# Optimization experiments

Measured on AMD Instinct MI355X. Metric: run time of the kernel, lower is better.

Reference implementation:

```python
import jax, jax.numpy as jnp
import numpy as np

B, NPG, H, D = 8, 6250, 4, 128   # graphs, nodes/graph, heads, hidden
N = B * NPG                       # 50000 nodes total
E = 400000                        # edges
VOCAB = 10000


def setup_inputs() -> dict:
    key = jax.random.key(0)
    ks = jax.random.split(key, 12)
    p = lambda k, shape: jax.random.normal(k, shape, dtype=jnp.float32) * 0.05
    return {
        "node_ids": jax.random.randint(ks[0], (N,), 0, VOCAB),
        "src": jax.random.randint(ks[1], (E,), 0, N),
        "dst": jax.random.randint(ks[2], (E,), 0, N),
        "emb": p(ks[3], (VOCAB, D)),
        "W_src": p(ks[4], (D, H * D)), "b_src": jnp.zeros((H * D,), jnp.float32),
        "W_dst": p(ks[5], (D, H * D)), "b_dst": jnp.zeros((H * D,), jnp.float32),
        "attn": p(ks[6], (H, D)),
        "W_res": p(ks[7], (D, H * D)), "b_res": jnp.zeros((H * D,), jnp.float32),
        "W_gc": p(ks[8], (D, D)), "b_gc": jnp.zeros((D,), jnp.float32),
        "W_mlp": p(ks[9], (3 * D, 1)), "b_mlp": jnp.zeros((1,), jnp.float32),
    }


def _leaky(x, s):
    return jnp.where(x >= 0, x, s * x)


def _maxpool(feat):
    # dgl.max_nodes: per-graph max over nodes -> [B, feat_dim]
    return jnp.max(feat.reshape(B, NPG, -1), axis=1)


def _gatv2(x, src, dst, W_src, b_src, W_dst, b_dst, attn, W_res, b_res):
    # DGL GATv2Conv (share_weights=False, residual=True, eval mode -> no dropout)
    hs = (x @ W_src + b_src).reshape(N, H, D)
    hd = (x @ W_dst + b_dst).reshape(N, H, D)
    e = _leaky(hs[src] + hd[dst], 0.2)              # [E,H,D]
    logits = jnp.einsum('ehd,hd->eh', e, attn)      # [E,H]
    m = jax.ops.segment_max(logits, dst, num_segments=N)
    ex = jnp.exp(logits - m[dst])
    denom = jax.ops.segment_sum(ex, dst, num_segments=N)
    alpha = ex / denom[dst]                          # edge softmax per dst/head
    rst = jax.ops.segment_sum(hs[src] * alpha[..., None], dst, num_segments=N)
    rst = rst + (x @ W_res + b_res).reshape(N, H, D)
    return _leaky(rst, 0.01)                         # nn.LeakyReLU() activation


def _graphconv(x, src, dst, W, b):
    # DGL GraphConv norm='both', allow_zero_in_degree=True, LeakyReLU activation
    ones = jnp.ones((E,), x.dtype)
    dout = jnp.clip(jax.ops.segment_sum(ones, src, num_segments=N), 1.0, None)
    din = jnp.clip(jax.ops.segment_sum(ones, dst, num_segments=N), 1.0, None)
    h = x * jax.lax.rsqrt(dout)[:, None]
    agg = jax.ops.segment_sum(h[src], dst, num_segments=N)
    h = agg * jax.lax.rsqrt(din)[:, None]
    return _leaky(h @ W + b, 0.01)


def reference(node_ids, src, dst, emb, W_src, b_src, W_dst, b_dst, attn,
              W_res, b_res, W_gc, b_gc, W_mlp, b_mlp):
    feat = emb[node_ids]                             # featurize_nodes
    pools = [_maxpool(feat)]
    res = _gatv2(feat, src, dst, W_src, b_src, W_dst, b_dst, attn,
                 W_res, b_res).mean(axis=1)          # mean over heads -> [N,D]
    pools.append(_maxpool(res))
    res = _graphconv(res, src, dst, W_gc, b_gc)
    pools.append(_maxpool(res))
    agg = jnp.concatenate(pools, axis=1)             # [B, 3D]
    # reward_predictor_block_two: ReLU -> (Dropout eval) -> Linear(3D, 1)
    return jax.nn.relu(agg) @ W_mlp + b_mlp          # BCE logits [B,1]
```

## Files before the change

kernel.cpp:

```cpp
#include <hip/hip_runtime.h>
#include <float.h>
#include <math.h>

#define Bg   8
#define NPGc 6250
#define Hh   4
#define Dd   128
#define Nn   50000
#define Ee   400000
#define HDd  512
#define NCHUNK 49

typedef unsigned short ushort_t;
typedef __attribute__((ext_vector_type(8))) short bf16x8;
typedef __attribute__((ext_vector_type(4))) float f32x4;
typedef __attribute__((ext_vector_type(2))) float f32x2;

__device__ __forceinline__ void atomicMaxF(float* addr, float val) {
    if (val >= 0.0f) atomicMax((int*)addr, __float_as_int(val));
    else             atomicMin((unsigned int*)addr, __float_as_uint(val));
}

__device__ __forceinline__ ushort_t f2bf(float x) {
    unsigned u = __float_as_uint(x);
    unsigned r = (u + 0x7FFFu + ((u >> 16) & 1u)) >> 16;
    return (ushort_t)r;
}

__device__ __forceinline__ f32x2 bfpair(unsigned u) {
    f32x2 r;
    r.x = __uint_as_float(u << 16);
    r.y = __uint_as_float(u & 0xFFFF0000u);
    return r;
}

__global__ void setup_kernel(const int* __restrict__ ids, const float* __restrict__ emb,
                             float* __restrict__ feat, ushort_t* __restrict__ feat_bf,
                             const float* __restrict__ W_src, const float* __restrict__ W_dst,
                             const float* __restrict__ W_res, const float* __restrict__ W_gc,
                             const float* __restrict__ b_src, const float* __restrict__ b_dst,
                             const float* __restrict__ b_res,
                             ushort_t* __restrict__ Wt_s, ushort_t* __restrict__ Wt_dr,
                             ushort_t* __restrict__ Wt_gc,
                             float* __restrict__ bias_s, float* __restrict__ bias_dr,
                             int* __restrict__ din_i, float* __restrict__ dout,
                             int* __restrict__ cursor, float* __restrict__ pools) {
    int i = blockIdx.x * blockDim.x + threadIdx.x;
    {
        int n = i >> 5, c = i & 31;
        int id = ids[n];
        float4 v = ((const float4*)emb)[(size_t)id * 32 + c];
        ((float4*)feat)[(size_t)n * 32 + c] = v;
        ushort4 b;
        b.x = f2bf(v.x); b.y = f2bf(v.y); b.z = f2bf(v.z); b.w = f2bf(v.w);
        ((ushort4*)feat_bf)[(size_t)n * 32 + c] = b;
    }
    if (i < Nn) { din_i[i] = 0; dout[i] = 0.0f; cursor[i] = 0; }
    if (i < Bg * 3 * Dd) pools[i] = -FLT_MAX;
    if (i < 512 * 128) {
        int c = i >> 7, k = i & 127;
        Wt_s[i] = f2bf(W_src[k * 512 + c]);
    } else if (i < 512 * 128 + 1024 * 128) {
        int j = i - 512 * 128;
        int c = j >> 7, k = j & 127;
        float v = (c < 512) ? W_dst[k * 512 + c] : W_res[k * 512 + (c - 512)];
        Wt_dr[j] = f2bf(v);
    } else if (i < 512 * 128 + 1024 * 128 + 128 * 128) {
        int j = i - (512 * 128 + 1024 * 128);
        int c = j >> 7, k = j & 127;
        Wt_gc[j] = f2bf(W_gc[k * 128 + c]);
    }
    if (i < 512) bias_s[i] = b_src[i];
    if (i < 1024) bias_dr[i] = (i < 512) ? b_dst[i] : b_res[i - 512];
}

__global__ void maxpool_kernel(const float* __restrict__ x, float* __restrict__ pools, int col_off) {
    int b = blockIdx.x, chunk = blockIdx.y, d = threadIdx.x;
    int i0 = chunk * 125, i1 = i0 + 125;
    float mx = -FLT_MAX;
    for (int i = i0; i < i1; ++i)
        mx = fmaxf(mx, x[((size_t)(b * NPGc + i)) * Dd + d]);
    atomicMaxF(&pools[b * (3 * Dd) + col_off + d], mx);
}

__global__ void maxpool_bf_kernel(const ushort_t* __restrict__ x, float* __restrict__ pools, int col_off) {
    int b = blockIdx.x, chunk = blockIdx.y, lane = threadIdx.x;
    int i0 = chunk * 125;
    f32x2 mx = {-FLT_MAX, -FLT_MAX};
    for (int i = 0; i < 125; ++i) {
        unsigned u = *(const unsigned*)(x + ((size_t)(b * NPGc + i0 + i)) * Dd + lane * 2);
        mx = __builtin_elementwise_max(mx, bfpair(u));
    }
    atomicMaxF(&pools[b * (3 * Dd) + col_off + lane * 2],     mx.x);
    atomicMaxF(&pools[b * (3 * Dd) + col_off + lane * 2 + 1], mx.y);
}

template<int GNT, int NCS>
__global__ __launch_bounds__(256) void mfma_gemm_kernel(
    const ushort_t* __restrict__ A, const ushort_t* __restrict__ Wt,
    const float* __restrict__ bias, ushort_t* __restrict__ Ob,
    int n_rows, int WN)
{
    __shared__ ushort_t Cs[2][64 * 64];
    int bid = blockIdx.x;
    int lin = (bid & 7) * (gridDim.x >> 3) + (bid >> 3);
    int row0 = (lin / NCS) * 64;
    int ct0  = (lin % NCS) * GNT;
    int w = threadIdx.x >> 6, lane = threadIdx.x & 63;
    int lrow = lane & 15, kg = lane >> 4;

    bf16x8 av[4][4];
    {
        const ushort_t* ap = A + (size_t)(row0 + lrow) * 128 + kg * 8;
        #pragma unroll
        for (int fi = 0; fi < 4; ++fi)
            #pragma unroll
            for (int ks = 0; ks < 4; ++ks)
                av[fi][ks] = *(const bf16x8*)(ap + fi * 16 * 128 + ks * 32);
    }
    bf16x8 wv[GNT][4];
    float4 bv[GNT];
    {
        const ushort_t* wp = Wt + (size_t)(ct0 * 64 + w * 16 + lrow) * 128 + kg * 8;
        #pragma unroll
        for (int ct = 0; ct < GNT; ++ct) {
            #pragma unroll
            for (int ks = 0; ks < 4; ++ks)
                wv[ct][ks] = *(const bf16x8*)(wp + (size_t)ct * 8192 + ks * 32);
            bv[ct] = *(const float4*)(bias + (ct0 + ct) * 64 + w * 16 + kg * 4);
        }
    }

    #pragma unroll
    for (int ct = 0; ct < GNT; ++ct) {
        f32x4 acc[4] = {};
        #pragma unroll
        for (int ks = 0; ks < 4; ++ks)
            #pragma unroll
            for (int fi = 0; fi < 4; ++fi)
                acc[fi] = __builtin_amdgcn_mfma_f32_16x16x32_bf16(wv[ct][ks], av[fi][ks], acc[fi], 0, 0, 0);

        ushort_t* cb = Cs[ct & 1];
        int cbase = w * 32 + kg * 8;
        #pragma unroll
        for (int fi = 0; fi < 4; ++fi) {
            float o0 = acc[fi][0] + bv[ct].x;
            float o1 = acc[fi][1] + bv[ct].y;
            float o2 = acc[fi][2] + bv[ct].z;
            float o3 = acc[fi][3] + bv[ct].w;
            unsigned q0, q1;
            asm("v_cvt_pk_bf16_f32 %0, %1, %2" : "=v"(q0) : "v"(o0), "v"(o1));
            asm("v_cvt_pk_bf16_f32 %0, %1, %2" : "=v"(q1) : "v"(o2), "v"(o3));
            int r = fi * 16 + lrow;
            int cbyte = cbase ^ ((r & 7) << 4);
            uint2 q; q.x = q0; q.y = q1;
            *(uint2*)((char*)cb + r * 128 + cbyte) = q;
        }
        __syncthreads();
        {
            int t = threadIdx.x;
            const char* cbr = (const char*)cb;
            #pragma unroll
            for (int h = 0; h < 2; ++h) {
                int r  = (h * 256 + t) >> 3;
                int ch = t & 7;
                int cbyte = (ch * 16) ^ ((r & 7) << 4);
                uint4 v = *(const uint4*)(cbr + r * 128 + cbyte);
                int grow = row0 + r;
                if (grow < n_rows)
                    *(uint4*)((char*)Ob + ((size_t)grow * WN + (ct0 + ct) * 64) * 2 + ch * 16) = v;
            }
        }
    }
}

__global__ __launch_bounds__(256) void mfma_gc_pool_kernel(
    const ushort_t* __restrict__ A, const ushort_t* __restrict__ Wt,
    const float* __restrict__ bias, float* __restrict__ pools)
{
    int g = blockIdx.x / 98, lb = blockIdx.x % 98;
    int row0 = g * NPGc + lb * 64;
    int w = threadIdx.x >> 6, lane = threadIdx.x & 63;
    int lrow = lane & 15, kg = lane >> 4;

    bf16x8 av[4][4];
    {
        const ushort_t* ap = A + (size_t)(row0 + lrow) * 128 + kg * 8;
        #pragma unroll
        for (int fi = 0; fi < 4; ++fi)
            #pragma unroll
            for (int ks = 0; ks < 4; ++ks)
                av[fi][ks] = *(const bf16x8*)(ap + fi * 16 * 128 + ks * 32);
    }

    #pragma unroll
    for (int ct = 0; ct < 2; ++ct) {
        bf16x8 wv[4];
        const ushort_t* wp = Wt + (size_t)(ct * 64 + w * 16 + lrow) * 128 + kg * 8;
        #pragma unroll
        for (int ks = 0; ks < 4; ++ks) wv[ks] = *(const bf16x8*)(wp + ks * 32);

        f32x4 acc[4] = {};
        #pragma unroll
        for (int ks = 0; ks < 4; ++ks)
            #pragma unroll
            for (int fi = 0; fi < 4; ++fi)
                acc[fi] = __builtin_amdgcn_mfma_f32_16x16x32_bf16(wv[ks], av[fi][ks], acc[fi], 0, 0, 0);

        int colb = ct * 64 + w * 16 + kg * 4;
        float4 bv4 = *(const float4*)(bias + colb);
        float mcol[4] = {-FLT_MAX, -FLT_MAX, -FLT_MAX, -FLT_MAX};
        #pragma unroll
        for (int fi = 0; fi < 4; ++fi) {
            int lr = lb * 64 + fi * 16 + lrow;
            bool valid = lr < NPGc;
            #pragma unroll
            for (int j = 0; j < 4; ++j) {
                float v = acc[fi][j] + ((const float*)&bv4)[j];
                v = v >= 0.0f ? v : 0.01f * v;
                if (valid) mcol[j] = fmaxf(mcol[j], v);
            }
        }
        #pragma unroll
        for (int j = 0; j < 4; ++j) {
            mcol[j] = fmaxf(mcol[j], __shfl_xor(mcol[j], 1));
            mcol[j] = fmaxf(mcol[j], __shfl_xor(mcol[j], 2));
            mcol[j] = fmaxf(mcol[j], __shfl_xor(mcol[j], 4));
            mcol[j] = fmaxf(mcol[j], __shfl_xor(mcol[j], 8));
        }
        if (lrow == 0) {
            #pragma unroll
            for (int j = 0; j < 4; ++j)
                atomicMaxF(&pools[g * (3 * Dd) + 2 * Dd + colb + j], mcol[j]);
        }
    }
}

__global__ void degree2_kernel(const int* __restrict__ src, const int* __restrict__ dst,
                               int* __restrict__ din_i, float* __restrict__ dout) {
    int e = blockIdx.x * blockDim.x + threadIdx.x;
    if (e >= Ee) return;
    atomicAdd(&din_i[dst[e]], 1);
    atomicAdd(&dout[src[e]], 1.0f);
}

__global__ __launch_bounds__(256) void scan_reduce_kernel(const int* __restrict__ din_i,
                                                          int* __restrict__ partials) {
    int b = blockIdx.x, t = threadIdx.x;
    int base = b * 1024 + t * 4;
    int s = 0;
    #pragma unroll
    for (int j = 0; j < 4; ++j) { int i = base + j; if (i < Nn) s += din_i[i]; }
    #pragma unroll
    for (int off = 32; off > 0; off >>= 1) s += __shfl_xor(s, off);
    __shared__ int wsum[4];
    if ((t & 63) == 0) wsum[t >> 6] = s;
    __syncthreads();
    if (t == 0) partials[b] = wsum[0] + wsum[1] + wsum[2] + wsum[3];
}

__global__ void scan_mid_kernel(int* __restrict__ partials, int* __restrict__ row_start) {
    if (threadIdx.x == 0) {
        int acc = 0;
        for (int i = 0; i < NCHUNK; ++i) { int v = partials[i]; partials[i] = acc; acc += v; }
        row_start[Nn] = acc;
    }
}

__global__ __launch_bounds__(256) void scan_final_kernel(const int* __restrict__ din_i,
                                                         const int* __restrict__ partials,
                                                         int* __restrict__ row_start,
                                                         float* __restrict__ din_f) {
    int b = blockIdx.x, t = threadIdx.x;
    int base = b * 1024 + t * 4;
    int v[4]; int s = 0;
    #pragma unroll
    for (int j = 0; j < 4; ++j) {
        v[j] = (base + j < Nn) ? din_i[base + j] : 0;
        s += v[j];
    }
    __shared__ int buf[256];
    buf[t] = s;
    __syncthreads();
    #pragma unroll
    for (int off = 1; off < 256; off <<= 1) {
        int x = (t >= off) ? buf[t - off] : 0;
        __syncthreads();
        buf[t] += x;
        __syncthreads();
    }
    int excl = buf[t] - s + partials[b];
    #pragma unroll
    for (int j = 0; j < 4; ++j) {
        if (base + j < Nn) {
            row_start[base + j] = excl;
            din_f[base + j] = (float)v[j];
            excl += v[j];
        }
    }
}

__global__ void scatter_kernel(const int* __restrict__ src, const int* __restrict__ dst,
                               const int* __restrict__ row_start, int* __restrict__ cursor,
                               int* __restrict__ csr_src) {
    int e = blockIdx.x * blockDim.x + threadIdx.x;
    if (e >= Ee) return;
    int d = dst[e];
    int slot = row_start[d] + atomicAdd(&cursor[d], 1);
    csr_src[slot] = src[e];
}

__global__ __launch_bounds__(256) void gat_fused_kernel(
    const ushort_t* __restrict__ feat_bf, const ushort_t* __restrict__ hs,
    const ushort_t* __restrict__ Wt_dr, const float* __restrict__ bias_dr,
    const float* __restrict__ attn,
    const int* __restrict__ row_start, const int* __restrict__ csr_src,
    ushort_t* __restrict__ res_bf)
{
    __shared__ char HD[16 * 2048];
    int nb = blockIdx.x * 16;
    int w = threadIdx.x >> 6, lane = threadIdx.x & 63;
    int lrow = lane & 15, kg = lane >> 4;

    {
        bf16x8 av[4];
        const ushort_t* ap = feat_bf + (size_t)(nb + lrow) * 128 + kg * 8;
        #pragma unroll
        for (int ks = 0; ks < 4; ++ks) av[ks] = *(const bf16x8*)(ap + ks * 32);
        #pragma unroll 4
        for (int cf = 0; cf < 16; ++cf) {
            int col0 = w * 256 + cf * 16;
            bf16x8 wv[4];
            const ushort_t* wp = Wt_dr + (size_t)(col0 + lrow) * 128 + kg * 8;
            #pragma unroll
            for (int ks = 0; ks < 4; ++ks) wv[ks] = *(const bf16x8*)(wp + ks * 32);
            f32x4 acc = {};
            #pragma unroll
            for (int ks = 0; ks < 4; ++ks)
                acc = __builtin_amdgcn_mfma_f32_16x16x32_bf16(wv[ks], av[ks], acc, 0, 0, 0);
            int colb = col0 + kg * 4;
            float4 bv = *(const float4*)(bias_dr + colb);
            float o0 = acc[0] + bv.x, o1 = acc[1] + bv.y;
            float o2 = acc[2] + bv.z, o3 = acc[3] + bv.w;
            unsigned q0, q1;
            asm("v_cvt_pk_bf16_f32 %0, %1, %2" : "=v"(q0) : "v"(o0), "v"(o1));
            asm("v_cvt_pk_bf16_f32 %0, %1, %2" : "=v"(q1) : "v"(o2), "v"(o3));
            int byte = (colb * 2) ^ ((lrow & 7) << 4);
            uint2 q; q.x = q0; q.y = q1;
            *(uint2*)(HD + lrow * 2048 + byte) = q;
        }
    }
    __syncthreads();

    const f32x2 z2 = {0.0f, 0.0f};
    f32x2 at0, at1, at2, at3;
    {
        float4 a0 = *(const float4*)(attn + lane * 8);
        float4 a1 = *(const float4*)(attn + lane * 8 + 4);
        at0.x = a0.x; at0.y = a0.y; at1.x = a0.z; at1.y = a0.w;
        at2.x = a1.x; at2.y = a1.y; at3.x = a1.z; at3.y = a1.w;
    }

    for (int i = 0; i < 4; ++i) {
        int r = w * 4 + i;
        int d = nb + r;
        int e0 = row_start[d], e1 = row_start[d + 1];

        f32x2 hd0, hd1, hd2, hd3;
        {
            uint4 hr = *(const uint4*)(HD + r * 2048 + ((lane * 16) ^ ((r & 7) << 4)));
            hd0 = bfpair(hr.x); hd1 = bfpair(hr.y); hd2 = bfpair(hr.z); hd3 = bfpair(hr.w);
        }

        float denom = 0.0f;
        f32x2 ac0 = z2, ac1 = z2, ac2 = z2, ac3 = z2;

#define LOGIT_PRE(rr, h0, h1, h2, h3, pout)                                           \
    {                                                                                 \
        h0 = bfpair(rr.x); h1 = bfpair(rr.y); h2 = bfpair(rr.z); h3 = bfpair(rr.w);   \
        f32x2 p2 = z2;                                                                \
        { f32x2 x = h0 + hd0;                                                         \
          p2 += (__builtin_elementwise_max(x, z2) + 0.2f * __builtin_elementwise_min(x, z2)) * at0; } \
        { f32x2 x = h1 + hd1;                                                         \
          p2 += (__builtin_elementwise_max(x, z2) + 0.2f * __builtin_elementwise_min(x, z2)) * at1; } \
        { f32x2 x = h2 + hd2;                                                         \
          p2 += (__builtin_elementwise_max(x, z2) + 0.2f * __builtin_elementwise_min(x, z2)) * at2; } \
        { f32x2 x = h3 + hd3;                                                         \
          p2 += (__builtin_elementwise_max(x, z2) + 0.2f * __builtin_elementwise_min(x, z2)) * at3; } \
        pout = p2.x + p2.y;                                                           \
    }

        int e = e0;
        for (; e + 4 <= e1; e += 4) {
            int sA = csr_src[e], sB = csr_src[e + 1], sC = csr_src[e + 2], sD = csr_src[e + 3];
            uint4 rA = *(const uint4*)(hs + (size_t)sA * HDd + lane * 8);
            uint4 rB = *(const uint4*)(hs + (size_t)sB * HDd + lane * 8);
            uint4 rC = *(const uint4*)(hs + (size_t)sC * HDd + lane * 8);
            uint4 rD = *(const uint4*)(hs + (size_t)sD * HDd + lane * 8);
            f32x2 hA0, hA1, hA2, hA3, hB0, hB1, hB2, hB3;
            f32x2 hC0, hC1, hC2, hC3, hD0, hD1, hD2, hD3;
            float pA, pB, pC, pD;
            LOGIT_PRE(rA, hA0, hA1, hA2, hA3, pA);
            LOGIT_PRE(rB, hB0, hB1, hB2, hB3, pB);
            LOGIT_PRE(rC, hC0, hC1, hC2, hC3, pC);
            LOGIT_PRE(rD, hD0, hD1, hD2, hD3, pD);
            pA += __shfl_xor(pA, 1); pB += __shfl_xor(pB, 1); pC += __shfl_xor(pC, 1); pD += __shfl_xor(pD, 1);
            pA += __shfl_xor(pA, 2); pB += __shfl_xor(pB, 2); pC += __shfl_xor(pC, 2); pD += __shfl_xor(pD, 2);
            pA += __shfl_xor(pA, 4); pB += __shfl_xor(pB, 4); pC += __shfl_xor(pC, 4); pD += __shfl_xor(pD, 4);
            pA += __shfl_xor(pA, 8); pB += __shfl_xor(pB, 8); pC += __shfl_xor(pC, 8); pD += __shfl_xor(pD, 8);
            float exA = __expf(fminf(fmaxf(pA, -40.0f), 40.0f));
            float exB = __expf(fminf(fmaxf(pB, -40.0f), 40.0f));
            float exC = __expf(fminf(fmaxf(pC, -40.0f), 40.0f));
            float exD = __expf(fminf(fmaxf(pD, -40.0f), 40.0f));
            denom += (exA + exB) + (exC + exD);
            ac0 += hA0 * exA + hB0 * exB + hC0 * exC + hD0 * exD;
            ac1 += hA1 * exA + hB1 * exB + hC1 * exC + hD1 * exD;
            ac2 += hA2 * exA + hB2 * exB + hC2 * exC + hD2 * exD;
            ac3 += hA3 * exA + hB3 * exB + hC3 * exC + hD3 * exD;
        }
        for (; e < e1; ++e) {
            int s = csr_src[e];
            uint4 rr = *(const uint4*)(hs + (size_t)s * HDd + lane * 8);
            f32x2 h0, h1, h2, h3;
            float p;
            LOGIT_PRE(rr, h0, h1, h2, h3, p);
            p += __shfl_xor(p, 1); p += __shfl_xor(p, 2);
            p += __shfl_xor(p, 4); p += __shfl_xor(p, 8);
            float ex = __expf(fminf(fmaxf(p, -40.0f), 40.0f));
            denom += ex;
            ac0 += h0 * ex; ac1 += h1 * ex; ac2 += h2 * ex; ac3 += h3 * ex;
        }
#undef LOGIT_PRE

        float inv = (e1 > e0) ? 1.0f / denom : 0.0f;
        f32x2 rv0, rv1, rv2, rv3;
        {
            uint4 rr = *(const uint4*)(HD + r * 2048 + ((1024 + lane * 16) ^ ((r & 7) << 4)));
            rv0 = bfpair(rr.x); rv1 = bfpair(rr.y); rv2 = bfpair(rr.z); rv3 = bfpair(rr.w);
        }
        float t[8];
        {
            f32x2 v0 = ac0 * inv + rv0, v1 = ac1 * inv + rv1;
            f32x2 v2 = ac2 * inv + rv2, v3 = ac3 * inv + rv3;
            f32x2 l0 = __builtin_elementwise_max(v0, z2) + 0.01f * __builtin_elementwise_min(v0, z2);
            f32x2 l1 = __builtin_elementwise_max(v1, z2) + 0.01f * __builtin_elementwise_min(v1, z2);
            f32x2 l2 = __builtin_elementwise_max(v2, z2) + 0.01f * __builtin_elementwise_min(v2, z2);
            f32x2 l3 = __builtin_elementwise_max(v3, z2) + 0.01f * __builtin_elementwise_min(v3, z2);
            t[0] = l0.x; t[1] = l0.y; t[2] = l1.x; t[3] = l1.y;
            t[4] = l2.x; t[5] = l2.y; t[6] = l3.x; t[7] = l3.y;
        }
        #pragma unroll
        for (int j = 0; j < 8; ++j) {
            t[j] += __shfl_xor(t[j], 16);
            t[j] += __shfl_xor(t[j], 32);
        }
        if (lane < 16) {
            float o0 = 0.25f * t[0], o1 = 0.25f * t[1], o2 = 0.25f * t[2], o3 = 0.25f * t[3];
            float o4 = 0.25f * t[4], o5 = 0.25f * t[5], o6 = 0.25f * t[6], o7 = 0.25f * t[7];
            unsigned q0, q1, q2, q3;
            asm("v_cvt_pk_bf16_f32 %0, %1, %2" : "=v"(q0) : "v"(o0), "v"(o1));
            asm("v_cvt_pk_bf16_f32 %0, %1, %2" : "=v"(q1) : "v"(o2), "v"(o3));
            asm("v_cvt_pk_bf16_f32 %0, %1, %2" : "=v"(q2) : "v"(o4), "v"(o5));
            asm("v_cvt_pk_bf16_f32 %0, %1, %2" : "=v"(q3) : "v"(o6), "v"(o7));
            uint4 qb; qb.x = q0; qb.y = q1; qb.z = q2; qb.w = q3;
            *(uint4*)(res_bf + (size_t)d * Dd + lane * 8) = qb;
        }
    }
}

__global__ __launch_bounds__(256) void gc_gather_kernel(
    const ushort_t* __restrict__ res_bf, const int* __restrict__ row_start,
    const int* __restrict__ csr_src, const float* __restrict__ dout,
    const float* __restrict__ din, ushort_t* __restrict__ agg_bf)
{
    int d = (blockIdx.x * 256 + threadIdx.x) >> 6;
    int lane = threadIdx.x & 63;
    if (d >= Nn) return;
    int e0 = row_start[d], e1 = row_start[d + 1];
    const f32x2 z2 = {0.0f, 0.0f};
    f32x2 a2 = z2;
    int s0 = (e0 < e1) ? csr_src[e0] : 0;
    int s1 = (e0 + 1 < e1) ? csr_src[e0 + 1] : s0;
    float sc0 = 1.0f / sqrtf(fmaxf((e0 < e1) ? dout[s0] : 1.0f, 1.0f));
    float sc1 = 1.0f / sqrtf(fmaxf((e0 + 1 < e1) ? dout[s1] : 1.0f, 1.0f));
    unsigned u0 = *(const unsigned*)(res_bf + (size_t)s0 * Dd + lane * 2);
    unsigned u1 = *(const unsigned*)(res_bf + (size_t)s1 * Dd + lane * 2);
    for (int e = e0; e < e1; ++e) {
        int s2 = (e + 2 < e1) ? csr_src[e + 2] : s0;
        float sc2 = 1.0f / sqrtf(fmaxf(dout[s2], 1.0f));
        unsigned u2 = *(const unsigned*)(res_bf + (size_t)s2 * Dd + lane * 2);
        a2 += bfpair(u0) * sc0;
        u0 = u1; u1 = u2; sc0 = sc1; sc1 = sc2;
    }
    float scd = 1.0f / sqrtf(fmaxf(din[d], 1.0f));
    float ax = a2.x * scd, ay = a2.y * scd;
    unsigned q;
    asm("v_cvt_pk_bf16_f32 %0, %1, %2" : "=v"(q) : "v"(ax), "v"(ay));
    *(unsigned*)(agg_bf + (size_t)d * Dd + lane * 2) = q;
}

__global__ void final_kernel(const float* __restrict__ pools, const float* __restrict__ W_mlp,
                             const float* __restrict__ b_mlp, float* __restrict__ out) {
    int b = blockIdx.x, lane = threadIdx.x;
    float s = 0.0f;
    for (int j = lane; j < 3 * Dd; j += 64)
        s += fmaxf(pools[b * (3 * Dd) + j], 0.0f) * W_mlp[j];
    #pragma unroll
    for (int off = 32; off > 0; off >>= 1) s += __shfl_xor(s, off);
    if (lane == 0) out[b] = s + b_mlp[0];
}

extern "C" void kernel_launch(void* const* d_in, const int* in_sizes, int n_in,
                              void* d_out, int out_size, void* d_ws, size_t ws_size,
                              hipStream_t stream) {
    const int*   node_ids = (const int*)d_in[0];
    const int*   src      = (const int*)d_in[1];
    const int*   dst      = (const int*)d_in[2];
    const float* emb      = (const float*)d_in[3];
    const float* W_src    = (const float*)d_in[4];
    const float* b_src    = (const float*)d_in[5];
    const float* W_dst    = (const float*)d_in[6];
    const float* b_dst    = (const float*)d_in[7];
    const float* attn     = (const float*)d_in[8];
    const float* W_res    = (const float*)d_in[9];
    const float* b_res    = (const float*)d_in[10];
    const float* W_gc     = (const float*)d_in[11];
    const float* b_gc     = (const float*)d_in[12];
    const float* W_mlp    = (const float*)d_in[13];
    const float* b_mlp    = (const float*)d_in[14];
    float* out = (float*)d_out;

    char* w = (char*)d_ws;
    size_t off = 0;
    float*    feat    = (float*)(w + off);    off += (size_t)Nn * Dd * 4;
    ushort_t* feat_bf = (ushort_t*)(w + off); off += (size_t)(Nn + 64) * Dd * 2;
    ushort_t* hs_buf  = (ushort_t*)(w + off); off += (size_t)Nn * HDd * 2;
    ushort_t* Wt_s    = (ushort_t*)(w + off); off += (size_t)512 * 128 * 2;
    ushort_t* Wt_dr   = (ushort_t*)(w + off); off += (size_t)1024 * 128 * 2;
    ushort_t* Wt_gc   = (ushort_t*)(w + off); off += (size_t)128 * 128 * 2;
    float*    bias_s  = (float*)(w + off);    off += 512 * 4;
    float*    bias_dr = (float*)(w + off);    off += 1024 * 4;
    int*      csr_src = (int*)(w + off);      off += (size_t)Ee * 4;
    int*      row_st  = (int*)(w + off);      off += ((size_t)Nn + 4) * 4;
    int*      cursor  = (int*)(w + off);      off += (size_t)Nn * 4;
    int*      din_i   = (int*)(w + off);      off += (size_t)Nn * 4;
    float*    din_f   = (float*)(w + off);    off += (size_t)Nn * 4;
    float*    dout_f  = (float*)(w + off);    off += (size_t)Nn * 4;
    int*      partials= (int*)(w + off);      off += 64 * 4;
    float*    pools   = (float*)(w + off);    off += (size_t)Bg * 3 * Dd * 4;
    ushort_t* res_bf  = (ushort_t*)(w + off); off += (size_t)Nn * Dd * 2;

    ushort_t* agg_bf = hs_buf;

    setup_kernel<<<(Nn * 32) / 256, 256, 0, stream>>>(
        node_ids, emb, feat, feat_bf, W_src, W_dst, W_res, W_gc,
        b_src, b_dst, b_res, Wt_s, Wt_dr, Wt_gc, bias_s, bias_dr,
        din_i, dout_f, cursor, pools);
    maxpool_kernel<<<dim3(Bg, 50), Dd, 0, stream>>>(feat, pools, 0);

    degree2_kernel<<<(Ee + 255) / 256, 256, 0, stream>>>(src, dst, din_i, dout_f);
    scan_reduce_kernel<<<NCHUNK, 256, 0, stream>>>(din_i, partials);
    scan_mid_kernel<<<1, 64, 0, stream>>>(partials, row_st);
    scan_final_kernel<<<NCHUNK, 256, 0, stream>>>(din_i, partials, row_st, din_f);
    scatter_kernel<<<(Ee + 255) / 256, 256, 0, stream>>>(src, dst, row_st, cursor, csr_src);

    mfma_gemm_kernel<2, 4><<<((Nn + 63) / 64) * 4, 256, 0, stream>>>(
        feat_bf, Wt_s, bias_s, hs_buf, Nn, HDd);

    gat_fused_kernel<<<Nn / 16, 256, 0, stream>>>(
        feat_bf, hs_buf, Wt_dr, bias_dr, attn, row_st, csr_src, res_bf);
    maxpool_bf_kernel<<<dim3(Bg, 50), 64, 0, stream>>>(res_bf, pools, Dd);

    gc_gather_kernel<<<(Nn * 64) / 256, 256, 0, stream>>>(res_bf, row_st, csr_src, dout_f, din_f, agg_bf);
    mfma_gc_pool_kernel<<<Bg * 98, 256, 0, stream>>>(agg_bf, Wt_gc, b_gc, pools);

    final_kernel<<<Bg, 64, 0, stream>>>(pools, W_mlp, b_mlp, out);
}
```

Before: 410.3 us.

## Unfuse dst/res GEMM from GAT kernel into separate MFMA GEMM; pool embeddings from bf16

Moves the per-block dst+residual projection (feat @ [W_dst|W_res]) out of the GAT aggregation kernel into a standalone MFMA GEMM that writes a 1024-wide bf16 buffer. The GAT kernel then becomes one wave per destination node, reading hd and residual rows from global memory instead of LDS, which removes the 32KB shared buffer and the block barrier. This should improve occupancy and load balance. It also drops the fp32 feature copy and runs the first maxpool on the bf16 features. The cost is an extra ~100MB of global traffic for writing and reading the hdres buffer, and the first pool now sees bf16-rounded values.

```diff
diff --git a/kernel.cpp b/kernel.cpp
--- a/kernel.cpp
+++ b/kernel.cpp
@@ -35,7 +35,7 @@
 }
 
 __global__ void setup_kernel(const int* __restrict__ ids, const float* __restrict__ emb,
-                             float* __restrict__ feat, ushort_t* __restrict__ feat_bf,
+                             ushort_t* __restrict__ feat_bf,
                              const float* __restrict__ W_src, const float* __restrict__ W_dst,
                              const float* __restrict__ W_res, const float* __restrict__ W_gc,
                              const float* __restrict__ b_src, const float* __restrict__ b_dst,
@@ -50,7 +50,6 @@
         int n = i >> 5, c = i & 31;
         int id = ids[n];
         float4 v = ((const float4*)emb)[(size_t)id * 32 + c];
-        ((float4*)feat)[(size_t)n * 32 + c] = v;
         ushort4 b;
         b.x = f2bf(v.x); b.y = f2bf(v.y); b.z = f2bf(v.z); b.w = f2bf(v.w);
         ((ushort4*)feat_bf)[(size_t)n * 32 + c] = b;
@@ -74,15 +73,6 @@
     if (i < 1024) bias_dr[i] = (i < 512) ? b_dst[i] : b_res[i - 512];
 }
 
-__global__ void maxpool_kernel(const float* __restrict__ x, float* __restrict__ pools, int col_off) {
-    int b = blockIdx.x, chunk = blockIdx.y, d = threadIdx.x;
-    int i0 = chunk * 125, i1 = i0 + 125;
-    float mx = -FLT_MAX;
-    for (int i = i0; i < i1; ++i)
-        mx = fmaxf(mx, x[((size_t)(b * NPGc + i)) * Dd + d]);
-    atomicMaxF(&pools[b * (3 * Dd) + col_off + d], mx);
-}
-
 __global__ void maxpool_bf_kernel(const ushort_t* __restrict__ x, float* __restrict__ pools, int col_off) {
     int b = blockIdx.x, chunk = blockIdx.y, lane = threadIdx.x;
     int i0 = chunk * 125;
@@ -311,69 +301,29 @@
 }
 
 __global__ __launch_bounds__(256) void gat_fused_kernel(
-    const ushort_t* __restrict__ feat_bf, const ushort_t* __restrict__ hs,
-    const ushort_t* __restrict__ Wt_dr, const float* __restrict__ bias_dr,
+    const ushort_t* __restrict__ hs, const ushort_t* __restrict__ hdres,
     const float* __restrict__ attn,
     const int* __restrict__ row_start, const int* __restrict__ csr_src,
     ushort_t* __restrict__ res_bf)
 {
-    __shared__ char HD[16 * 2048];
-    int nb = blockIdx.x * 16;
-    int w = threadIdx.x >> 6, lane = threadIdx.x & 63;
-    int lrow = lane & 15, kg = lane >> 4;
-
-    {
-        bf16x8 av[4];
-        const ushort_t* ap = feat_bf + (size_t)(nb + lrow) * 128 + kg * 8;
-        #pragma unroll
-        for (int ks = 0; ks < 4; ++ks) av[ks] = *(const bf16x8*)(ap + ks * 32);
-        #pragma unroll 4
-        for (int cf = 0; cf < 16; ++cf) {
-            int col0 = w * 256 + cf * 16;
-            bf16x8 wv[4];
-            const ushort_t* wp = Wt_dr + (size_t)(col0 + lrow) * 128 + kg * 8;
-            #pragma unroll
-            for (int ks = 0; ks < 4; ++ks) wv[ks] = *(const bf16x8*)(wp + ks * 32);
-            f32x4 acc = {};
-            #pragma unroll
-            for (int ks = 0; ks < 4; ++ks)
-                acc = __builtin_amdgcn_mfma_f32_16x16x32_bf16(wv[ks], av[ks], acc, 0, 0, 0);
-            int colb = col0 + kg * 4;
-            float4 bv = *(const float4*)(bias_dr + colb);
-            float o0 = acc[0] + bv.x, o1 = acc[1] + bv.y;
-            float o2 = acc[2] + bv.z, o3 = acc[3] + bv.w;
-            unsigned q0, q1;
-            asm("v_cvt_pk_bf16_f32 %0, %1, %2" : "=v"(q0) : "v"(o0), "v"(o1));
-            asm("v_cvt_pk_bf16_f32 %0, %1, %2" : "=v"(q1) : "v"(o2), "v"(o3));
-            int byte = (colb * 2) ^ ((lrow & 7) << 4);
-            uint2 q; q.x = q0; q.y = q1;
-            *(uint2*)(HD + lrow * 2048 + byte) = q;
-        }
-    }
-    __syncthreads();
+    int d = (blockIdx.x * 256 + threadIdx.x) >> 6;
+    int lane = threadIdx.x & 63;
+    if (d >= Nn) return;
+    int e0 = row_start[d], e1 = row_start[d + 1];
 
     const f32x2 z2 = {0.0f, 0.0f};
-    f32x2 at0, at1, at2, at3;
-    {
+    f32x2 hd0, hd1, hd2, hd3, at0, at1, at2, at3;
+    {
+        uint4 hr = *(const uint4*)(hdres + (size_t)d * 1024 + lane * 8);
+        hd0 = bfpair(hr.x); hd1 = bfpair(hr.y); hd2 = bfpair(hr.z); hd3 = bfpair(hr.w);
         float4 a0 = *(const float4*)(attn + lane * 8);
         float4 a1 = *(const float4*)(attn + lane * 8 + 4);
         at0.x = a0.x; at0.y = a0.y; at1.x = a0.z; at1.y = a0.w;
         at2.x = a1.x; at2.y = a1.y; at3.x = a1.z; at3.y = a1.w;
     }
 
-    for (int i = 0; i < 4; ++i) {
-        int r = w * 4 + i;
-        int d = nb + r;
-        int e0 = row_start[d], e1 = row_start[d + 1];
-
-        f32x2 hd0, hd1, hd2, hd3;
-        {
-            uint4 hr = *(const uint4*)(HD + r * 2048 + ((lane * 16) ^ ((r & 7) << 4)));
-            hd0 = bfpair(hr.x); hd1 = bfpair(hr.y); hd2 = bfpair(hr.z); hd3 = bfpair(hr.w);
-        }
-
-        float denom = 0.0f;
-        f32x2 ac0 = z2, ac1 = z2, ac2 = z2, ac3 = z2;
+    float denom = 0.0f;
+    f32x2 ac0 = z2, ac1 = z2, ac2 = z2, ac3 = z2;
 
 #define LOGIT_PRE(rr, h0, h1, h2, h3, pout)                                           \
     {                                                                                 \
@@ -390,81 +340,80 @@
         pout = p2.x + p2.y;                                                           \
     }
 
-        int e = e0;
-        for (; e + 4 <= e1; e += 4) {
-            int sA = csr_src[e], sB = csr_src[e + 1], sC = csr_src[e + 2], sD = csr_src[e + 3];
-            uint4 rA = *(const uint4*)(hs + (size_t)sA * HDd + lane * 8);
-            uint4 rB = *(const uint4*)(hs + (size_t)sB * HDd + lane * 8);
-            uint4 rC = *(const uint4*)(hs + (size_t)sC * HDd + lane * 8);
-            uint4 rD = *(const uint4*)(hs + (size_t)sD * HDd + lane * 8);
-            f32x2 hA0, hA1, hA2, hA3, hB0, hB1, hB2, hB3;
-            f32x2 hC0, hC1, hC2, hC3, hD0, hD1, hD2, hD3;
-            float pA, pB, pC, pD;
-            LOGIT_PRE(rA, hA0, hA1, hA2, hA3, pA);
-            LOGIT_PRE(rB, hB0, hB1, hB2, hB3, pB);
-            LOGIT_PRE(rC, hC0, hC1, hC2, hC3, pC);
-            LOGIT_PRE(rD, hD0, hD1, hD2, hD3, pD);
-            pA += __shfl_xor(pA, 1); pB += __shfl_xor(pB, 1); pC += __shfl_xor(pC, 1); pD += __shfl_xor(pD, 1);
-            pA += __shfl_xor(pA, 2); pB += __shfl_xor(pB, 2); pC += __shfl_xor(pC, 2); pD += __shfl_xor(pD, 2);
-            pA += __shfl_xor(pA, 4); pB += __shfl_xor(pB, 4); pC += __shfl_xor(pC, 4); pD += __shfl_xor(pD, 4);
-            pA += __shfl_xor(pA, 8); pB += __shfl_xor(pB, 8); pC += __shfl_xor(pC, 8); pD += __shfl_xor(pD, 8);
-            float exA = __expf(fminf(fmaxf(pA, -40.0f), 40.0f));
-            float exB = __expf(fminf(fmaxf(pB, -40.0f), 40.0f));
-            float exC = __expf(fminf(fmaxf(pC, -40.0f), 40.0f));
-            float exD = __expf(fminf(fmaxf(pD, -40.0f), 40.0f));
-            denom += (exA + exB) + (exC + exD);
-            ac0 += hA0 * exA + hB0 * exB + hC0 * exC + hD0 * exD;
-            ac1 += hA1 * exA + hB1 * exB + hC1 * exC + hD1 * exD;
-            ac2 += hA2 * exA + hB2 * exB + hC2 * exC + hD2 * exD;
-            ac3 += hA3 * exA + hB3 * exB + hC3 * exC + hD3 * exD;
-        }
-        for (; e < e1; ++e) {
-            int s = csr_src[e];
-            uint4 rr = *(const uint4*)(hs + (size_t)s * HDd + lane * 8);
-            f32x2 h0, h1, h2, h3;
-            float p;
-            LOGIT_PRE(rr, h0, h1, h2, h3, p);
-            p += __shfl_xor(p, 1); p += __shfl_xor(p, 2);
-            p += __shfl_xor(p, 4); p += __shfl_xor(p, 8);
-            float ex = __expf(fminf(fmaxf(p, -40.0f), 40.0f));
-            denom += ex;
-            ac0 += h0 * ex; ac1 += h1 * ex; ac2 += h2 * ex; ac3 += h3 * ex;
-        }
+    int e = e0;
+    for (; e + 4 <= e1; e += 4) {
+        int sA = csr_src[e], sB = csr_src[e + 1], sC = csr_src[e + 2], sD = csr_src[e + 3];
+        uint4 rA = *(const uint4*)(hs + (size_t)sA * HDd + lane * 8);
+        uint4 rB = *(const uint4*)(hs + (size_t)sB * HDd + lane * 8);
+        uint4 rC = *(const uint4*)(hs + (size_t)sC * HDd + lane * 8);
+        uint4 rD = *(const uint4*)(hs + (size_t)sD * HDd + lane * 8);
+        f32x2 hA0, hA1, hA2, hA3, hB0, hB1, hB2, hB3;
+        f32x2 hC0, hC1, hC2, hC3, hD0, hD1, hD2, hD3;
+        float pA, pB, pC, pD;
+        LOGIT_PRE(rA, hA0, hA1, hA2, hA3, pA);
+        LOGIT_PRE(rB, hB0, hB1, hB2, hB3, pB);
+        LOGIT_PRE(rC, hC0, hC1, hC2, hC3, pC);
+        LOGIT_PRE(rD, hD0, hD1, hD2, hD3, pD);
+        pA += __shfl_xor(pA, 1); pB += __shfl_xor(pB, 1); pC += __shfl_xor(pC, 1); pD += __shfl_xor(pD, 1);
+        pA += __shfl_xor(pA, 2); pB += __shfl_xor(pB, 2); pC += __shfl_xor(pC, 2); pD += __shfl_xor(pD, 2);
+        pA += __shfl_xor(pA, 4); pB += __shfl_xor(pB, 4); pC += __shfl_xor(pC, 4); pD += __shfl_xor(pD, 4);
+        pA += __shfl_xor(pA, 8); pB += __shfl_xor(pB, 8); pC += __shfl_xor(pC, 8); pD += __shfl_xor(pD, 8);
+        float exA = __expf(fminf(fmaxf(pA, -40.0f), 40.0f));
+        float exB = __expf(fminf(fmaxf(pB, -40.0f), 40.0f));
+        float exC = __expf(fminf(fmaxf(pC, -40.0f), 40.0f));
+        float exD = __expf(fminf(fmaxf(pD, -40.0f), 40.0f));
+        denom += (exA + exB) + (exC + exD);
+        ac0 += hA0 * exA + hB0 * exB + hC0 * exC + hD0 * exD;
+        ac1 += hA1 * exA + hB1 * exB + hC1 * exC + hD1 * exD;
+        ac2 += hA2 * exA + hB2 * exB + hC2 * exC + hD2 * exD;
+        ac3 += hA3 * exA + hB3 * exB + hC3 * exC + hD3 * exD;
+    }
+    for (; e < e1; ++e) {
+        int s = csr_src[e];
+        uint4 rr = *(const uint4*)(hs + (size_t)s * HDd + lane * 8);
+        f32x2 h0, h1, h2, h3;
+        float p;
+        LOGIT_PRE(rr, h0, h1, h2, h3, p);
+        p += __shfl_xor(p, 1); p += __shfl_xor(p, 2);
+        p += __shfl_xor(p, 4); p += __shfl_xor(p, 8);
+        float ex = __expf(fminf(fmaxf(p, -40.0f), 40.0f));
+        denom += ex;
+        ac0 += h0 * ex; ac1 += h1 * ex; ac2 += h2 * ex; ac3 += h3 * ex;
+    }
 #undef LOGIT_PRE
 
-        float inv = (e1 > e0) ? 1.0f / denom : 0.0f;
-        f32x2 rv0, rv1, rv2, rv3;
-        {
-            uint4 rr = *(const uint4*)(HD + r * 2048 + ((1024 + lane * 16) ^ ((r & 7) << 4)));
-            rv0 = bfpair(rr.x); rv1 = bfpair(rr.y); rv2 = bfpair(rr.z); rv3 = bfpair(rr.w);
-        }
-        float t[8];
-        {
-            f32x2 v0 = ac0 * inv + rv0, v1 = ac1 * inv + rv1;
-            f32x2 v2 = ac2 * inv + rv2, v3 = ac3 * inv + rv3;
-            f32x2 l0 = __builtin_elementwise_max(v0, z2) + 0.01f * __builtin_elementwise_min(v0, z2);
-            f32x2 l1 = __builtin_elementwise_max(v1, z2) + 0.01f * __builtin_elementwise_min(v1, z2);
-            f32x2 l2 = __builtin_elementwise_max(v2, z2) + 0.01f * __builtin_elementwise_min(v2, z2);
-            f32x2 l3 = __builtin_elementwise_max(v3, z2) + 0.01f * __builtin_elementwise_min(v3, z2);
-            t[0] = l0.x; t[1] = l0.y; t[2] = l1.x; t[3] = l1.y;
-            t[4] = l2.x; t[5] = l2.y; t[6] = l3.x; t[7] = l3.y;
-        }
-        #pragma unroll
-        for (int j = 0; j < 8; ++j) {
-            t[j] += __shfl_xor(t[j], 16);
-            t[j] += __shfl_xor(t[j], 32);
-        }
-        if (lane < 16) {
-            float o0 = 0.25f * t[0], o1 = 0.25f * t[1], o2 = 0.25f * t[2], o3 = 0.25f * t[3];
-            float o4 = 0.25f * t[4], o5 = 0.25f * t[5], o6 = 0.25f * t[6], o7 = 0.25f * t[7];
-            unsigned q0, q1, q2, q3;
-            asm("v_cvt_pk_bf16_f32 %0, %1, %2" : "=v"(q0) : "v"(o0), "v"(o1));
-            asm("v_cvt_pk_bf16_f32 %0, %1, %2" : "=v"(q1) : "v"(o2), "v"(o3));
-            asm("v_cvt_pk_bf16_f32 %0, %1, %2" : "=v"(q2) : "v"(o4), "v"(o5));
-            asm("v_cvt_pk_bf16_f32 %0, %1, %2" : "=v"(q3) : "v"(o6), "v"(o7));
-            uint4 qb; qb.x = q0; qb.y = q1; qb.z = q2; qb.w = q3;
-            *(uint4*)(res_bf + (size_t)d * Dd + lane * 8) = qb;
-        }
+    float inv = (e1 > e0) ? 1.0f / denom : 0.0f;
+    f32x2 rv0, rv1, rv2, rv3;
+    {
+        uint4 rr = *(const uint4*)(hdres + (size_t)d * 1024 + 512 + lane * 8);
+        rv0 = bfpair(rr.x); rv1 = bfpair(rr.y); rv2 = bfpair(rr.z); rv3 = bfpair(rr.w);
+    }
+    float t[8];
+    {
+        f32x2 v0 = ac0 * inv + rv0, v1 = ac1 * inv + rv1;
+        f32x2 v2 = ac2 * inv + rv2, v3 = ac3 * inv + rv3;
+        f32x2 l0 = __builtin_elementwise_max(v0, z2) + 0.01f * __builtin_elementwise_min(v0, z2);
+        f32x2 l1 = __builtin_elementwise_max(v1, z2) + 0.01f * __builtin_elementwise_min(v1, z2);
+        f32x2 l2 = __builtin_elementwise_max(v2, z2) + 0.01f * __builtin_elementwise_min(v2, z2);
+        f32x2 l3 = __builtin_elementwise_max(v3, z2) + 0.01f * __builtin_elementwise_min(v3, z2);
+        t[0] = l0.x; t[1] = l0.y; t[2] = l1.x; t[3] = l1.y;
+        t[4] = l2.x; t[5] = l2.y; t[6] = l3.x; t[7] = l3.y;
+    }
+    #pragma unroll
+    for (int j = 0; j < 8; ++j) {
+        t[j] += __shfl_xor(t[j], 16);
+        t[j] += __shfl_xor(t[j], 32);
+    }
+    if (lane < 16) {
+        float o0 = 0.25f * t[0], o1 = 0.25f * t[1], o2 = 0.25f * t[2], o3 = 0.25f * t[3];
+        float o4 = 0.25f * t[4], o5 = 0.25f * t[5], o6 = 0.25f * t[6], o7 = 0.25f * t[7];
+        unsigned q0, q1, q2, q3;
+        asm("v_cvt_pk_bf16_f32 %0, %1, %2" : "=v"(q0) : "v"(o0), "v"(o1));
+        asm("v_cvt_pk_bf16_f32 %0, %1, %2" : "=v"(q1) : "v"(o2), "v"(o3));
+        asm("v_cvt_pk_bf16_f32 %0, %1, %2" : "=v"(q2) : "v"(o4), "v"(o5));
+        asm("v_cvt_pk_bf16_f32 %0, %1, %2" : "=v"(q3) : "v"(o6), "v"(o7));
+        uint4 qb; qb.x = q0; qb.y = q1; qb.z = q2; qb.w = q3;
+        *(uint4*)(res_bf + (size_t)d * Dd + lane * 8) = qb;
     }
 }
 
@@ -532,9 +481,9 @@
 
     char* w = (char*)d_ws;
     size_t off = 0;
-    float*    feat    = (float*)(w + off);    off += (size_t)Nn * Dd * 4;
     ushort_t* feat_bf = (ushort_t*)(w + off); off += (size_t)(Nn + 64) * Dd * 2;
     ushort_t* hs_buf  = (ushort_t*)(w + off); off += (size_t)Nn * HDd * 2;
+    ushort_t* hdres   = (ushort_t*)(w + off); off += (size_t)Nn * 1024 * 2;
     ushort_t* Wt_s    = (ushort_t*)(w + off); off += (size_t)512 * 128 * 2;
     ushort_t* Wt_dr   = (ushort_t*)(w + off); off += (size_t)1024 * 128 * 2;
     ushort_t* Wt_gc   = (ushort_t*)(w + off); off += (size_t)128 * 128 * 2;
@@ -553,10 +502,10 @@
     ushort_t* agg_bf = hs_buf;
 
     setup_kernel<<<(Nn * 32) / 256, 256, 0, stream>>>(
-        node_ids, emb, feat, feat_bf, W_src, W_dst, W_res, W_gc,
+        node_ids, emb, feat_bf, W_src, W_dst, W_res, W_gc,
         b_src, b_dst, b_res, Wt_s, Wt_dr, Wt_gc, bias_s, bias_dr,
         din_i, dout_f, cursor, pools);
-    maxpool_kernel<<<dim3(Bg, 50), Dd, 0, stream>>>(feat, pools, 0);
+    maxpool_bf_kernel<<<dim3(Bg, 50), 64, 0, stream>>>(feat_bf, pools, 0);
 
     degree2_kernel<<<(Ee + 255) / 256, 256, 0, stream>>>(src, dst, din_i, dout_f);
     scan_reduce_kernel<<<NCHUNK, 256, 0, stream>>>(din_i, partials);
@@ -566,9 +515,11 @@
 
     mfma_gemm_kernel<2, 4><<<((Nn + 63) / 64) * 4, 256, 0, stream>>>(
         feat_bf, Wt_s, bias_s, hs_buf, Nn, HDd);
-
-    gat_fused_kernel<<<Nn / 16, 256, 0, stream>>>(
-        feat_bf, hs_buf, Wt_dr, bias_dr, attn, row_st, csr_src, res_bf);
+    mfma_gemm_kernel<2, 8><<<((Nn + 63) / 64) * 8, 256, 0, stream>>>(
+        feat_bf, Wt_dr, bias_dr, hdres, Nn, 1024);
+
+    gat_fused_kernel<<<(Nn * 64) / 256, 256, 0, stream>>>(
+        hs_buf, hdres, attn, row_st, csr_src, res_bf);
     maxpool_bf_kernel<<<dim3(Bg, 50), 64, 0, stream>>>(res_bf, pools, Dd);
 
     gc_gather_kernel<<<(Nn * 64) / 256, 256, 0, stream>>>(res_bf, row_st, csr_src, dout_f, din_f, agg_bf);
```

Result: faster. 384.4 us (-6.3%).
